# Kernel tuning notes

Measured on AMD Instinct MI355X. Metric: run time of the kernel, lower is better.

## Reference

```python
import jax, jax.numpy as jnp
import numpy as np

TOP_K = 2

def _moe_forward(x, gate_w, w1, w2, w3):
    # x: [B,S,H] -> tokens [T,H]
    B, S, H = x.shape
    xt = x.reshape(-1, H)                              # [T,H]
    T = xt.shape[0]
    E = gate_w.shape[0]
    # router
    logits = xt @ gate_w.T                             # [T,E]
    probs = jax.nn.softmax(logits.astype(jnp.float32), axis=-1)
    rw, sel = jax.lax.top_k(probs, TOP_K)              # [T,K]
    rw = rw / jnp.sum(rw, axis=-1, keepdims=True)
    # per-token per-expert combine weight (0 if expert not selected)
    combine = jnp.zeros((T, E), dtype=xt.dtype).at[
        jnp.arange(T)[:, None], sel].add(rw.astype(xt.dtype))  # [T,E]
    # dense per-expert SwiGLU FFN over all tokens (prefill path of module)
    h1 = jnp.einsum('th,efh->tef', xt, w1)             # [T,E,F]
    h3 = jnp.einsum('th,efh->tef', xt, w3)             # [T,E,F]
    g = jax.nn.silu(h1) * h3                           # [T,E,F]
    g = g * combine[:, :, None]                        # apply routing weight before down-proj
    out = jnp.einsum('tef,ehf->th', g, w2)             # [T,H]
    return out.reshape(B, S, H)


def setup_inputs() -> dict:
    key = jax.random.key(0)
    ks = jax.random.split(key, 5)
    B, S, H, F, E = 2, 2048, 1024, 3584, 8
    scale = 1.0 / np.sqrt(H)
    return {
        'hidden_states': jax.random.normal(ks[0], (B, S, H), jnp.float32),
        'gate_w': jax.random.normal(ks[1], (E, H), jnp.float32) * scale,
        'w1': jax.random.normal(ks[2], (E, F, H), jnp.float32) * scale,
        'w2': jax.random.normal(ks[3], (E, H, F), jnp.float32) * (1.0 / np.sqrt(F)),
        'w3': jax.random.normal(ks[4], (E, F, H), jnp.float32) * scale,
    }


def reference(hidden_states, gate_w, w1, w2, w3):
    return _moe_forward(hidden_states, gate_w, w1, w2, w3)
```

## Files before the change

kernel.cpp:

```cpp
#include <hip/hip_runtime.h>
#include <hip/hip_bf16.h>

#define TT   4096
#define HH   1024
#define FF   3584
#define EE   8
#define N13  7168
#define TKP  8192

#define BM 128
#define BN 128
#define BK 64
#define LDK 72

typedef unsigned short u16;
typedef __attribute__((ext_vector_type(8))) short short8;
typedef __attribute__((ext_vector_type(4))) float floatx4;

__device__ __forceinline__ u16 f2b(float f) {
  union { float f; unsigned u; } v; v.f = f;
  unsigned r = v.u + 0x7FFFu + ((v.u >> 16) & 1u);
  return (u16)(r >> 16);
}
__device__ __forceinline__ float b2f(u16 u) {
  union { unsigned u; float f; } v; v.u = ((unsigned)u) << 16; return v.f;
}
__device__ __forceinline__ float blo(unsigned u) {
  union { unsigned u; float f; } v; v.u = u << 16; return v.f;
}
__device__ __forceinline__ float bhi(unsigned u) {
  union { unsigned u; float f; } v; v.u = u & 0xFFFF0000u; return v.f;
}

__global__ __launch_bounds__(256) void cvt_x(const float4* __restrict__ in, ushort4* __restrict__ outp) {
  int i = blockIdx.x * 256 + threadIdx.x;
  float4 v = in[i];
  ushort4 o; o.x = f2b(v.x); o.y = f2b(v.y); o.z = f2b(v.z); o.w = f2b(v.w);
  outp[i] = o;
}

__global__ __launch_bounds__(256) void cvt_w13(const float* __restrict__ w1, const float* __restrict__ w3,
                                               ushort4* __restrict__ w13b) {
  int i = blockIdx.x * 256 + threadIdx.x;
  const int perE = N13 * (HH / 4);
  int e = i / perE;
  int rem = i - e * perE;
  int n = rem / (HH / 4);
  int h4 = rem - n * (HH / 4);
  const float4* src = (n < FF)
      ? ((const float4*)(w1 + (size_t)(e * FF + n) * HH)) + h4
      : ((const float4*)(w3 + (size_t)(e * FF + (n - FF)) * HH)) + h4;
  float4 v = *src;
  ushort4 o; o.x = f2b(v.x); o.y = f2b(v.y); o.z = f2b(v.z); o.w = f2b(v.w);
  w13b[i] = o;
}

__global__ __launch_bounds__(256) void cvt_w2(const float4* __restrict__ in, ushort4* __restrict__ outp) {
  int i = blockIdx.x * 256 + threadIdx.x;
  float4 v = in[i];
  ushort4 o; o.x = f2b(v.x); o.y = f2b(v.y); o.z = f2b(v.z); o.w = f2b(v.w);
  outp[i] = o;
}

__global__ __launch_bounds__(256) void router(const float* __restrict__ x, const float* __restrict__ gw,
                                              int* __restrict__ cnt, int* __restrict__ tok_list,
                                              float* __restrict__ wt_list) {
  int lane = threadIdx.x & 63;
  int wv = threadIdx.x >> 6;
  int t = blockIdx.x * 4 + wv;
  const float* xp = x + (size_t)t * HH;
  float acc[EE];
#pragma unroll
  for (int e = 0; e < EE; e++) acc[e] = 0.f;
  for (int h = lane; h < HH; h += 64) {
    float xv = xp[h];
#pragma unroll
    for (int e = 0; e < EE; e++) acc[e] += xv * gw[e * HH + h];
  }
#pragma unroll
  for (int e = 0; e < EE; e++) {
#pragma unroll
    for (int off = 32; off > 0; off >>= 1) acc[e] += __shfl_xor(acc[e], off, 64);
  }
  if (lane == 0) {
    int i1 = 0;
#pragma unroll
    for (int e = 1; e < EE; e++) if (acc[e] > acc[i1]) i1 = e;
    int i2 = -1;
#pragma unroll
    for (int e = 0; e < EE; e++) {
      if (e == i1) continue;
      if (i2 < 0 || acc[e] > acc[i2]) i2 = e;
    }
    float wA = 1.f / (1.f + __expf(acc[i2] - acc[i1]));
    float wB = 1.f - wA;
    int p1 = atomicAdd(cnt + i1, 1);
    tok_list[i1 * TT + p1] = t; wt_list[i1 * TT + p1] = wA;
    int p2 = atomicAdd(cnt + i2, 1);
    tok_list[i2 * TT + p2] = t; wt_list[i2 * TT + p2] = wB;
  }
}

__global__ void mk_offsets(const int* __restrict__ cnt, int* __restrict__ offs) {
  if (threadIdx.x == 0) {
    int s = 0;
    for (int e = 0; e < EE; e++) { offs[e] = s; s += cnt[e]; }
  }
}

__global__ __launch_bounds__(256) void pairmap(const int* __restrict__ cnt, const int* __restrict__ offs,
                                               const int* __restrict__ tok_list, const float* __restrict__ wt_list,
                                               int* __restrict__ tokp, float* __restrict__ wtp) {
  int i = blockIdx.x * 256 + threadIdx.x;
  int e = i >> 12;
  int s = i & (TT - 1);
  if (s < cnt[e]) {
    int p = offs[e] + s;
    tokp[p] = tok_list[i];
    wtp[p] = wt_list[i];
  }
}

__global__ __launch_bounds__(256) void gemm_a(const u16* __restrict__ xb, const u16* __restrict__ w13b,
                                              const int* __restrict__ cnt, const int* __restrict__ offs,
                                              const int* __restrict__ tok_list, u16* __restrict__ h13) {
  const int ntile = blockIdx.x;
  const int e = blockIdx.y >> 5;
  const int rt = blockIdx.y & 31;
  const int cn = cnt[e];
  if (rt * BM >= cn) return;

  __shared__ u16 As[BM][LDK];
  __shared__ u16 Bs[BN][LDK];
  __shared__ int toks[BM];

  const int tid = threadIdx.x;
  if (tid < BM) {
    int r = rt * BM + tid;
    if (r >= cn) r = cn - 1;
    toks[tid] = tok_list[e * TT + r];
  }
  __syncthreads();

  const int r0 = tid >> 3;
  const int c0 = (tid & 7) * 8;
  const u16* aptr[4];
  const u16* bptr[4];
#pragma unroll
  for (int i = 0; i < 4; i++) {
    int r = r0 + i * 32;
    aptr[i] = xb + (size_t)toks[r] * HH + c0;
    bptr[i] = w13b + ((size_t)e * N13 + (size_t)ntile * BN + r) * HH + c0;
  }

  const int lane = tid & 63;
  const int wv = tid >> 6;
  const int wr = (wv >> 1) * 64;
  const int wc = (wv & 1) * 64;
  const int fr = lane & 15;
  const int fk = (lane >> 4) * 8;

  floatx4 acc[4][4];
#pragma unroll
  for (int mi = 0; mi < 4; mi++)
#pragma unroll
    for (int ni = 0; ni < 4; ni++)
#pragma unroll
      for (int q = 0; q < 4; q++) acc[mi][ni][q] = 0.f;

  for (int k0 = 0; k0 < HH; k0 += BK) {
#pragma unroll
    for (int i = 0; i < 4; i++) {
      uint4 av = *(const uint4*)(aptr[i]); aptr[i] += BK;
      uint4 bv = *(const uint4*)(bptr[i]); bptr[i] += BK;
      *(uint4*)&As[r0 + i * 32][c0] = av;
      *(uint4*)&Bs[r0 + i * 32][c0] = bv;
    }
    __syncthreads();
#pragma unroll
    for (int ks = 0; ks < 2; ks++) {
      short8 af[4], bfr[4];
#pragma unroll
      for (int mi = 0; mi < 4; mi++) af[mi] = *(const short8*)&As[wr + mi * 16 + fr][ks * 32 + fk];
#pragma unroll
      for (int ni = 0; ni < 4; ni++) bfr[ni] = *(const short8*)&Bs[wc + ni * 16 + fr][ks * 32 + fk];
#pragma unroll
      for (int mi = 0; mi < 4; mi++)
#pragma unroll
        for (int ni = 0; ni < 4; ni++)
          acc[mi][ni] = __builtin_amdgcn_mfma_f32_16x16x32_bf16(af[mi], bfr[ni], acc[mi][ni], 0, 0, 0);
    }
    __syncthreads();
  }

  const int gofs = offs[e];
#pragma unroll
  for (int mi = 0; mi < 4; mi++) {
#pragma unroll
    for (int i = 0; i < 4; i++) {
      int r = wr + mi * 16 + (lane >> 4) * 4 + i;
      int gr = rt * BM + r;
      if (gr < cn) {
        u16* dst = h13 + (size_t)(gofs + gr) * N13 + (size_t)ntile * BN + wc + (lane & 15);
#pragma unroll
        for (int ni = 0; ni < 4; ni++) dst[ni * 16] = f2b(acc[mi][ni][i]);
      }
    }
  }
}

__global__ __launch_bounds__(256) void silu_k(const u16* __restrict__ h13, const float* __restrict__ wtp,
                                              u16* __restrict__ g) {
  int i = blockIdx.x * 256 + threadIdx.x;
  int p = i / (FF / 8);
  int f8 = i - p * (FF / 8);
  const u16* row = h13 + (size_t)p * N13 + f8 * 8;
  uint4 va = *(const uint4*)(row);
  uint4 vb = *(const uint4*)(row + FF);
  float w = wtp[p];
  unsigned ua[4] = {va.x, va.y, va.z, va.w};
  unsigned ub[4] = {vb.x, vb.y, vb.z, vb.w};
  unsigned uo[4];
#pragma unroll
  for (int j = 0; j < 4; j++) {
    float a0 = blo(ua[j]), a1 = bhi(ua[j]);
    float b0 = blo(ub[j]), b1 = bhi(ub[j]);
    float s0 = a0 / (1.f + __expf(-a0));
    float s1 = a1 / (1.f + __expf(-a1));
    u16 o0 = f2b(s0 * b0 * w);
    u16 o1 = f2b(s1 * b1 * w);
    uo[j] = (unsigned)o0 | ((unsigned)o1 << 16);
  }
  uint4 vo; vo.x = uo[0]; vo.y = uo[1]; vo.z = uo[2]; vo.w = uo[3];
  *(uint4*)(g + (size_t)p * FF + f8 * 8) = vo;
}

__global__ __launch_bounds__(256) void gemm_b(const u16* __restrict__ g, const u16* __restrict__ w2b,
                                              const int* __restrict__ cnt, const int* __restrict__ offs,
                                              const int* __restrict__ tokp, float* __restrict__ out) {
  const int ntile = blockIdx.x;
  const int e = blockIdx.y >> 5;
  const int rt = blockIdx.y & 31;
  const int cn = cnt[e];
  if (rt * BM >= cn) return;
  const int gofs = offs[e];

  __shared__ u16 As[BM][LDK];
  __shared__ u16 Bs[BN][LDK];
  __shared__ int toks[BM];

  const int tid = threadIdx.x;
  if (tid < BM) {
    int r = rt * BM + tid;
    if (r >= cn) r = cn - 1;
    toks[tid] = tokp[gofs + r];
  }
  __syncthreads();

  const int r0 = tid >> 3;
  const int c0 = (tid & 7) * 8;
  const u16* aptr[4];
  const u16* bptr[4];
#pragma unroll
  for (int i = 0; i < 4; i++) {
    int r = r0 + i * 32;
    int gr = rt * BM + r;
    if (gr >= cn) gr = cn - 1;
    aptr[i] = g + (size_t)(gofs + gr) * FF + c0;
    bptr[i] = w2b + ((size_t)e * HH + (size_t)ntile * BN + r) * FF + c0;
  }

  const int lane = tid & 63;
  const int wv = tid >> 6;
  const int wr = (wv >> 1) * 64;
  const int wc = (wv & 1) * 64;
  const int fr = lane & 15;
  const int fk = (lane >> 4) * 8;

  floatx4 acc[4][4];
#pragma unroll
  for (int mi = 0; mi < 4; mi++)
#pragma unroll
    for (int ni = 0; ni < 4; ni++)
#pragma unroll
      for (int q = 0; q < 4; q++) acc[mi][ni][q] = 0.f;

  for (int k0 = 0; k0 < FF; k0 += BK) {
#pragma unroll
    for (int i = 0; i < 4; i++) {
      uint4 av = *(const uint4*)(aptr[i]); aptr[i] += BK;
      uint4 bv = *(const uint4*)(bptr[i]); bptr[i] += BK;
      *(uint4*)&As[r0 + i * 32][c0] = av;
      *(uint4*)&Bs[r0 + i * 32][c0] = bv;
    }
    __syncthreads();
#pragma unroll
    for (int ks = 0; ks < 2; ks++) {
      short8 af[4], bfr[4];
#pragma unroll
      for (int mi = 0; mi < 4; mi++) af[mi] = *(const short8*)&As[wr + mi * 16 + fr][ks * 32 + fk];
#pragma unroll
      for (int ni = 0; ni < 4; ni++) bfr[ni] = *(const short8*)&Bs[wc + ni * 16 + fr][ks * 32 + fk];
#pragma unroll
      for (int mi = 0; mi < 4; mi++)
#pragma unroll
        for (int ni = 0; ni < 4; ni++)
          acc[mi][ni] = __builtin_amdgcn_mfma_f32_16x16x32_bf16(af[mi], bfr[ni], acc[mi][ni], 0, 0, 0);
    }
    __syncthreads();
  }

#pragma unroll
  for (int mi = 0; mi < 4; mi++) {
#pragma unroll
    for (int i = 0; i < 4; i++) {
      int r = wr + mi * 16 + (lane >> 4) * 4 + i;
      int gr = rt * BM + r;
      if (gr < cn) {
        int tk = toks[r];
        float* dst = out + (size_t)tk * HH + (size_t)ntile * BN + wc + (lane & 15);
#pragma unroll
        for (int ni = 0; ni < 4; ni++) atomicAdd(dst + ni * 16, acc[mi][ni][i]);
      }
    }
  }
}

extern "C" void kernel_launch(void* const* d_in, const int* in_sizes, int n_in,
                              void* d_out, int out_size, void* d_ws, size_t ws_size,
                              hipStream_t stream) {
  const float* x  = (const float*)d_in[0];
  const float* gw = (const float*)d_in[1];
  const float* w1 = (const float*)d_in[2];
  const float* w2 = (const float*)d_in[3];
  const float* w3 = (const float*)d_in[4];
  float* out = (float*)d_out;

  char* ws = (char*)d_ws;
  u16* xb    = (u16*)ws;  ws += (size_t)TT * HH * 2;
  u16* w13b  = (u16*)ws;  ws += (size_t)EE * N13 * HH * 2;
  u16* w2b   = (u16*)ws;  ws += (size_t)EE * HH * FF * 2;
  u16* h13   = (u16*)ws;  ws += (size_t)TKP * N13 * 2;
  u16* gbuf  = (u16*)ws;  ws += (size_t)TKP * FF * 2;
  int* cnt   = (int*)ws;  ws += 256;
  int* offs  = (int*)ws;  ws += 256;
  int* tok_list = (int*)ws;   ws += (size_t)EE * TT * 4;
  float* wt_list = (float*)ws; ws += (size_t)EE * TT * 4;
  int* tokp  = (int*)ws;  ws += (size_t)TKP * 4;
  float* wtp = (float*)ws; ws += (size_t)TKP * 4;

  hipMemsetAsync(cnt, 0, 256, stream);
  hipMemsetAsync(out, 0, (size_t)TT * HH * 4, stream);

  cvt_x<<<(TT * HH / 4) / 256, 256, 0, stream>>>((const float4*)x, (ushort4*)xb);
  cvt_w13<<<(EE * N13 * (HH / 4)) / 256, 256, 0, stream>>>(w1, w3, (ushort4*)w13b);
  cvt_w2<<<(EE * HH * (FF / 4)) / 256, 256, 0, stream>>>((const float4*)w2, (ushort4*)w2b);

  router<<<TT / 4, 256, 0, stream>>>(x, gw, cnt, tok_list, wt_list);
  mk_offsets<<<1, 64, 0, stream>>>(cnt, offs);
  pairmap<<<(EE * TT) / 256, 256, 0, stream>>>(cnt, offs, tok_list, wt_list, tokp, wtp);

  gemm_a<<<dim3(N13 / BN, EE * (TT / BM)), 256, 0, stream>>>(xb, w13b, cnt, offs, tok_list, h13);
  silu_k<<<(TKP * (FF / 8)) / 256, 256, 0, stream>>>(h13, wtp, gbuf);
  gemm_b<<<dim3(HH / BN, EE * (TT / BM)), 256, 0, stream>>>(gbuf, w2b, cnt, offs, tokp, out);
}
```

Baseline: 858.5 us.

## Fuse SiLU gating into gate/up GEMM epilogue and use direct global-to-LDS loads

The w1/w3 rows are interleaved in 16-row groups so each gate/up GEMM tile holds matching h1 and h3 columns. SiLU, the multiply and the routing weight are then applied in the epilogue, which removes the h13 intermediate buffer and the separate silu kernel. Both GEMMs now use global_load_lds to move tiles straight into unpadded LDS with an XOR swizzle in place of row padding, cutting register traffic and bank conflicts. This adds swizzle and interleave index logic, and the fused epilogue issues scattered 2-byte stores.

```diff
diff --git a/kernel.cpp b/kernel.cpp
--- a/kernel.cpp
+++ b/kernel.cpp
@@ -11,7 +11,6 @@
 #define BM 128
 #define BN 128
 #define BK 64
-#define LDK 72
 
 typedef unsigned short u16;
 typedef __attribute__((ext_vector_type(8))) short short8;
@@ -22,14 +21,11 @@
   unsigned r = v.u + 0x7FFFu + ((v.u >> 16) & 1u);
   return (u16)(r >> 16);
 }
-__device__ __forceinline__ float b2f(u16 u) {
-  union { unsigned u; float f; } v; v.u = ((unsigned)u) << 16; return v.f;
-}
-__device__ __forceinline__ float blo(unsigned u) {
-  union { unsigned u; float f; } v; v.u = u << 16; return v.f;
-}
-__device__ __forceinline__ float bhi(unsigned u) {
-  union { unsigned u; float f; } v; v.u = u & 0xFFFF0000u; return v.f;
+
+__device__ __forceinline__ void gld_lds16(const u16* g, u16* l) {
+  __builtin_amdgcn_global_load_lds((const __attribute__((address_space(1))) unsigned int*)g,
+                                   (__attribute__((address_space(3))) unsigned int*)l,
+                                   16, 0, 0);
 }
 
 __global__ __launch_bounds__(256) void cvt_x(const float4* __restrict__ in, ushort4* __restrict__ outp) {
@@ -40,19 +36,20 @@
 }
 
 __global__ __launch_bounds__(256) void cvt_w13(const float* __restrict__ w1, const float* __restrict__ w3,
-                                               ushort4* __restrict__ w13b) {
+                                               ushort4* __restrict__ w13i) {
   int i = blockIdx.x * 256 + threadIdx.x;
   const int perE = N13 * (HH / 4);
   int e = i / perE;
   int rem = i - e * perE;
   int n = rem / (HH / 4);
   int h4 = rem - n * (HH / 4);
-  const float4* src = (n < FF)
-      ? ((const float4*)(w1 + (size_t)(e * FF + n) * HH)) + h4
-      : ((const float4*)(w3 + (size_t)(e * FF + (n - FF)) * HH)) + h4;
+  int f = ((n >> 5) << 4) + (n & 15);
+  int sel = (n >> 4) & 1;
+  const float* base = sel ? w3 : w1;
+  const float4* src = ((const float4*)(base + (size_t)(e * FF + f) * HH)) + h4;
   float4 v = *src;
   ushort4 o; o.x = f2b(v.x); o.y = f2b(v.y); o.z = f2b(v.z); o.w = f2b(v.w);
-  w13b[i] = o;
+  w13i[i] = o;
 }
 
 __global__ __launch_bounds__(256) void cvt_w2(const float4* __restrict__ in, ushort4* __restrict__ outp) {
@@ -109,48 +106,52 @@
 }
 
 __global__ __launch_bounds__(256) void pairmap(const int* __restrict__ cnt, const int* __restrict__ offs,
-                                               const int* __restrict__ tok_list, const float* __restrict__ wt_list,
-                                               int* __restrict__ tokp, float* __restrict__ wtp) {
+                                               const int* __restrict__ tok_list,
+                                               int* __restrict__ tokp) {
   int i = blockIdx.x * 256 + threadIdx.x;
   int e = i >> 12;
   int s = i & (TT - 1);
   if (s < cnt[e]) {
-    int p = offs[e] + s;
-    tokp[p] = tok_list[i];
-    wtp[p] = wt_list[i];
-  }
-}
-
-__global__ __launch_bounds__(256) void gemm_a(const u16* __restrict__ xb, const u16* __restrict__ w13b,
+    tokp[offs[e] + s] = tok_list[i];
+  }
+}
+
+__global__ __launch_bounds__(256) void gemm_a(const u16* __restrict__ xb, const u16* __restrict__ w13i,
                                               const int* __restrict__ cnt, const int* __restrict__ offs,
-                                              const int* __restrict__ tok_list, u16* __restrict__ h13) {
+                                              const int* __restrict__ tok_list, const float* __restrict__ wt_list,
+                                              u16* __restrict__ gbuf) {
   const int ntile = blockIdx.x;
   const int e = blockIdx.y >> 5;
   const int rt = blockIdx.y & 31;
   const int cn = cnt[e];
   if (rt * BM >= cn) return;
 
-  __shared__ u16 As[BM][LDK];
-  __shared__ u16 Bs[BN][LDK];
+  __shared__ u16 As[BM * BK];
+  __shared__ u16 Bs[BN * BK];
   __shared__ int toks[BM];
+  __shared__ float wts[BM];
 
   const int tid = threadIdx.x;
   if (tid < BM) {
     int r = rt * BM + tid;
     if (r >= cn) r = cn - 1;
     toks[tid] = tok_list[e * TT + r];
+    wts[tid] = wt_list[e * TT + r];
   }
   __syncthreads();
 
-  const int r0 = tid >> 3;
-  const int c0 = (tid & 7) * 8;
   const u16* aptr[4];
   const u16* bptr[4];
+  u16* alds[4];
+  u16* blds[4];
 #pragma unroll
   for (int i = 0; i < 4; i++) {
-    int r = r0 + i * 32;
-    aptr[i] = xb + (size_t)toks[r] * HH + c0;
-    bptr[i] = w13b + ((size_t)e * N13 + (size_t)ntile * BN + r) * HH + c0;
+    int row = (tid >> 3) + i * 32;
+    int c8 = (tid & 7) ^ (row & 7);
+    aptr[i] = xb + (size_t)toks[row] * HH + c8 * 8;
+    bptr[i] = w13i + ((size_t)e * N13 + (size_t)ntile * BN + row) * HH + c8 * 8;
+    alds[i] = As + row * BK + (tid & 7) * 8;
+    blds[i] = Bs + row * BK + (tid & 7) * 8;
   }
 
   const int lane = tid & 63;
@@ -158,7 +159,7 @@
   const int wr = (wv >> 1) * 64;
   const int wc = (wv & 1) * 64;
   const int fr = lane & 15;
-  const int fk = (lane >> 4) * 8;
+  const int fk8 = lane >> 4;
 
   floatx4 acc[4][4];
 #pragma unroll
@@ -171,19 +172,18 @@
   for (int k0 = 0; k0 < HH; k0 += BK) {
 #pragma unroll
     for (int i = 0; i < 4; i++) {
-      uint4 av = *(const uint4*)(aptr[i]); aptr[i] += BK;
-      uint4 bv = *(const uint4*)(bptr[i]); bptr[i] += BK;
-      *(uint4*)&As[r0 + i * 32][c0] = av;
-      *(uint4*)&Bs[r0 + i * 32][c0] = bv;
+      gld_lds16(aptr[i], alds[i]); aptr[i] += BK;
+      gld_lds16(bptr[i], blds[i]); bptr[i] += BK;
     }
     __syncthreads();
 #pragma unroll
     for (int ks = 0; ks < 2; ks++) {
+      int c8 = (ks * 4 + fk8) ^ (fr & 7);
       short8 af[4], bfr[4];
 #pragma unroll
-      for (int mi = 0; mi < 4; mi++) af[mi] = *(const short8*)&As[wr + mi * 16 + fr][ks * 32 + fk];
-#pragma unroll
-      for (int ni = 0; ni < 4; ni++) bfr[ni] = *(const short8*)&Bs[wc + ni * 16 + fr][ks * 32 + fk];
+      for (int mi = 0; mi < 4; mi++) af[mi] = *(const short8*)&As[(wr + mi * 16 + fr) * BK + c8 * 8];
+#pragma unroll
+      for (int ni = 0; ni < 4; ni++) bfr[ni] = *(const short8*)&Bs[(wc + ni * 16 + fr) * BK + c8 * 8];
 #pragma unroll
       for (int mi = 0; mi < 4; mi++)
 #pragma unroll
@@ -194,45 +194,26 @@
   }
 
   const int gofs = offs[e];
+  const int cl = lane & 15;
 #pragma unroll
   for (int mi = 0; mi < 4; mi++) {
 #pragma unroll
-    for (int i = 0; i < 4; i++) {
-      int r = wr + mi * 16 + (lane >> 4) * 4 + i;
+    for (int q = 0; q < 4; q++) {
+      int r = wr + mi * 16 + (lane >> 4) * 4 + q;
       int gr = rt * BM + r;
       if (gr < cn) {
-        u16* dst = h13 + (size_t)(gofs + gr) * N13 + (size_t)ntile * BN + wc + (lane & 15);
-#pragma unroll
-        for (int ni = 0; ni < 4; ni++) dst[ni * 16] = f2b(acc[mi][ni][i]);
+        float w = wts[r];
+        u16* dst = gbuf + (size_t)(gofs + gr) * FF + (size_t)ntile * 64 + wc / 2 + cl;
+#pragma unroll
+        for (int pg = 0; pg < 2; pg++) {
+          float h1 = acc[mi][2 * pg][q];
+          float h3 = acc[mi][2 * pg + 1][q];
+          float s = h1 / (1.f + __expf(-h1));
+          dst[pg * 16] = f2b(s * h3 * w);
+        }
       }
     }
   }
-}
-
-__global__ __launch_bounds__(256) void silu_k(const u16* __restrict__ h13, const float* __restrict__ wtp,
-                                              u16* __restrict__ g) {
-  int i = blockIdx.x * 256 + threadIdx.x;
-  int p = i / (FF / 8);
-  int f8 = i - p * (FF / 8);
-  const u16* row = h13 + (size_t)p * N13 + f8 * 8;
-  uint4 va = *(const uint4*)(row);
-  uint4 vb = *(const uint4*)(row + FF);
-  float w = wtp[p];
-  unsigned ua[4] = {va.x, va.y, va.z, va.w};
-  unsigned ub[4] = {vb.x, vb.y, vb.z, vb.w};
-  unsigned uo[4];
-#pragma unroll
-  for (int j = 0; j < 4; j++) {
-    float a0 = blo(ua[j]), a1 = bhi(ua[j]);
-    float b0 = blo(ub[j]), b1 = bhi(ub[j]);
-    float s0 = a0 / (1.f + __expf(-a0));
-    float s1 = a1 / (1.f + __expf(-a1));
-    u16 o0 = f2b(s0 * b0 * w);
-    u16 o1 = f2b(s1 * b1 * w);
-    uo[j] = (unsigned)o0 | ((unsigned)o1 << 16);
-  }
-  uint4 vo; vo.x = uo[0]; vo.y = uo[1]; vo.z = uo[2]; vo.w = uo[3];
-  *(uint4*)(g + (size_t)p * FF + f8 * 8) = vo;
 }
 
 __global__ __launch_bounds__(256) void gemm_b(const u16* __restrict__ g, const u16* __restrict__ w2b,
@@ -245,8 +226,8 @@
   if (rt * BM >= cn) return;
   const int gofs = offs[e];
 
-  __shared__ u16 As[BM][LDK];
-  __shared__ u16 Bs[BN][LDK];
+  __shared__ u16 As[BM * BK];
+  __shared__ u16 Bs[BN * BK];
   __shared__ int toks[BM];
 
   const int tid = threadIdx.x;
@@ -257,17 +238,20 @@
   }
   __syncthreads();
 
-  const int r0 = tid >> 3;
-  const int c0 = (tid & 7) * 8;
   const u16* aptr[4];
   const u16* bptr[4];
+  u16* alds[4];
+  u16* blds[4];
 #pragma unroll
   for (int i = 0; i < 4; i++) {
-    int r = r0 + i * 32;
-    int gr = rt * BM + r;
+    int row = (tid >> 3) + i * 32;
+    int gr = rt * BM + row;
     if (gr >= cn) gr = cn - 1;
-    aptr[i] = g + (size_t)(gofs + gr) * FF + c0;
-    bptr[i] = w2b + ((size_t)e * HH + (size_t)ntile * BN + r) * FF + c0;
+    int c8 = (tid & 7) ^ (row & 7);
+    aptr[i] = g + (size_t)(gofs + gr) * FF + c8 * 8;
+    bptr[i] = w2b + ((size_t)e * HH + (size_t)ntile * BN + row) * FF + c8 * 8;
+    alds[i] = As + row * BK + (tid & 7) * 8;
+    blds[i] = Bs + row * BK + (tid & 7) * 8;
   }
 
   const int lane = tid & 63;
@@ -275,7 +259,7 @@
   const int wr = (wv >> 1) * 64;
   const int wc = (wv & 1) * 64;
   const int fr = lane & 15;
-  const int fk = (lane >> 4) * 8;
+  const int fk8 = lane >> 4;
 
   floatx4 acc[4][4];
 #pragma unroll
@@ -288,19 +272,18 @@
   for (int k0 = 0; k0 < FF; k0 += BK) {
 #pragma unroll
     for (int i = 0; i < 4; i++) {
-      uint4 av = *(const uint4*)(aptr[i]); aptr[i] += BK;
-      uint4 bv = *(const uint4*)(bptr[i]); bptr[i] += BK;
-      *(uint4*)&As[r0 + i * 32][c0] = av;
-      *(uint4*)&Bs[r0 + i * 32][c0] = bv;
+      gld_lds16(aptr[i], alds[i]); aptr[i] += BK;
+      gld_lds16(bptr[i], blds[i]); bptr[i] += BK;
     }
     __syncthreads();
 #pragma unroll
     for (int ks = 0; ks < 2; ks++) {
+      int c8 = (ks * 4 + fk8) ^ (fr & 7);
       short8 af[4], bfr[4];
 #pragma unroll
-      for (int mi = 0; mi < 4; mi++) af[mi] = *(const short8*)&As[wr + mi * 16 + fr][ks * 32 + fk];
-#pragma unroll
-      for (int ni = 0; ni < 4; ni++) bfr[ni] = *(const short8*)&Bs[wc + ni * 16 + fr][ks * 32 + fk];
+      for (int mi = 0; mi < 4; mi++) af[mi] = *(const short8*)&As[(wr + mi * 16 + fr) * BK + c8 * 8];
+#pragma unroll
+      for (int ni = 0; ni < 4; ni++) bfr[ni] = *(const short8*)&Bs[(wc + ni * 16 + fr) * BK + c8 * 8];
 #pragma unroll
       for (int mi = 0; mi < 4; mi++)
 #pragma unroll
@@ -313,14 +296,14 @@
 #pragma unroll
   for (int mi = 0; mi < 4; mi++) {
 #pragma unroll
-    for (int i = 0; i < 4; i++) {
-      int r = wr + mi * 16 + (lane >> 4) * 4 + i;
+    for (int q = 0; q < 4; q++) {
+      int r = wr + mi * 16 + (lane >> 4) * 4 + q;
       int gr = rt * BM + r;
       if (gr < cn) {
         int tk = toks[r];
         float* dst = out + (size_t)tk * HH + (size_t)ntile * BN + wc + (lane & 15);
 #pragma unroll
-        for (int ni = 0; ni < 4; ni++) atomicAdd(dst + ni * 16, acc[mi][ni][i]);
+        for (int ni = 0; ni < 4; ni++) atomicAdd(dst + ni * 16, acc[mi][ni][q]);
       }
     }
   }
@@ -338,29 +321,26 @@
 
   char* ws = (char*)d_ws;
   u16* xb    = (u16*)ws;  ws += (size_t)TT * HH * 2;
-  u16* w13b  = (u16*)ws;  ws += (size_t)EE * N13 * HH * 2;
+  u16* w13i  = (u16*)ws;  ws += (size_t)EE * N13 * HH * 2;
   u16* w2b   = (u16*)ws;  ws += (size_t)EE * HH * FF * 2;
-  u16* h13   = (u16*)ws;  ws += (size_t)TKP * N13 * 2;
   u16* gbuf  = (u16*)ws;  ws += (size_t)TKP * FF * 2;
   int* cnt   = (int*)ws;  ws += 256;
   int* offs  = (int*)ws;  ws += 256;
   int* tok_list = (int*)ws;   ws += (size_t)EE * TT * 4;
   float* wt_list = (float*)ws; ws += (size_t)EE * TT * 4;
   int* tokp  = (int*)ws;  ws += (size_t)TKP * 4;
-  float* wtp = (float*)ws; ws += (size_t)TKP * 4;
 
   hipMemsetAsync(cnt, 0, 256, stream);
   hipMemsetAsync(out, 0, (size_t)TT * HH * 4, stream);
 
   cvt_x<<<(TT * HH / 4) / 256, 256, 0, stream>>>((const float4*)x, (ushort4*)xb);
-  cvt_w13<<<(EE * N13 * (HH / 4)) / 256, 256, 0, stream>>>(w1, w3, (ushort4*)w13b);
+  cvt_w13<<<(EE * N13 * (HH / 4)) / 256, 256, 0, stream>>>(w1, w3, (ushort4*)w13i);
   cvt_w2<<<(EE * HH * (FF / 4)) / 256, 256, 0, stream>>>((const float4*)w2, (ushort4*)w2b);
 
   router<<<TT / 4, 256, 0, stream>>>(x, gw, cnt, tok_list, wt_list);
   mk_offsets<<<1, 64, 0, stream>>>(cnt, offs);
-  pairmap<<<(EE * TT) / 256, 256, 0, stream>>>(cnt, offs, tok_list, wt_list, tokp, wtp);
-
-  gemm_a<<<dim3(N13 / BN, EE * (TT / BM)), 256, 0, stream>>>(xb, w13b, cnt, offs, tok_list, h13);
-  silu_k<<<(TKP * (FF / 8)) / 256, 256, 0, stream>>>(h13, wtp, gbuf);
+  pairmap<<<(EE * TT) / 256, 256, 0, stream>>>(cnt, offs, tok_list, tokp);
+
+  gemm_a<<<dim3(N13 / BN, EE * (TT / BM)), 256, 0, stream>>>(xb, w13i, cnt, offs, tok_list, wt_list, gbuf);
   gemm_b<<<dim3(HH / BN, EE * (TT / BM)), 256, 0, stream>>>(gbuf, w2b, cnt, offs, tokp, out);
 }
```

After: 738.2 us. 14.0% less time.
